# Kernel tuning notes

Hardware: AMD Instinct MI355X
Metric: run time of the kernel (lower is better)

## Reference

```python
import jax, jax.numpy as jnp
import numpy as np

B = 2_000_000
INPUT_DIM = 2
HIDDEN = 32
HALF = HIDDEN // 2  # 16
N_BUCKETS = 50


def setup_inputs() -> dict:
    key = jax.random.key(0)
    ks = jax.random.split(key, 8)
    x = jax.random.normal(ks[0], (B, INPUT_DIM), dtype=jnp.float32)
    buckets = jax.random.randint(ks[1], (B,), 0, N_BUCKETS)
    # shared MLP params (Linear stores W as [out,in]; we keep [in,out] for einsum)
    W1 = jax.random.normal(ks[2], (INPUT_DIM, HIDDEN), dtype=jnp.float32) * 0.5
    b1 = jax.random.normal(ks[3], (HIDDEN,), dtype=jnp.float32) * 0.1
    W2 = jax.random.normal(ks[4], (HIDDEN, HALF), dtype=jnp.float32) * 0.2
    b2 = jax.random.normal(ks[5], (HALF,), dtype=jnp.float32) * 0.1
    # per-bucket heads: each Linear(HALF, 1) -> stacked [N_BUCKETS, HALF] + [N_BUCKETS]
    Wh = jax.random.normal(ks[6], (N_BUCKETS, HALF), dtype=jnp.float32) * 0.2
    bh = jax.random.normal(ks[7], (N_BUCKETS,), dtype=jnp.float32) * 0.1
    return {"x": x, "buckets": buckets, "W1": W1, "b1": b1, "W2": W2, "b2": b2, "Wh": Wh, "bh": bh}


def reference(x, buckets, W1, b1, W2, b2, Wh, bh):
    # shared MLP: Linear -> ReLU -> Linear
    h = jax.nn.relu(x @ W1 + b1) @ W2 + b2            # [B, HALF]
    # bucket routing with clamp-to-last for out-of-range ids
    ids = jnp.where(buckets < N_BUCKETS, buckets, N_BUCKETS - 1)  # [B]
    w = Wh[ids]                                        # [B, HALF] gather
    out = jnp.einsum('bd,bd->b', h, w) + bh[ids]       # [B]
    return out
```

## Files before the change

kernel.cpp:

```cpp
#include <hip/hip_runtime.h>

#define NB 50
#define BLOCK 256


__device__ __forceinline__ float dot4relu(float x0, float x1,
                                          float4 wa, float4 wb, float4 bb,
                                          float4 v, float acc)
{
    float h;
    h = fmaf(x0, wa.x, fmaf(x1, wb.x, bb.x)); h = fmaxf(h, 0.f); acc = fmaf(h, v.x, acc);
    h = fmaf(x0, wa.y, fmaf(x1, wb.y, bb.y)); h = fmaxf(h, 0.f); acc = fmaf(h, v.y, acc);
    h = fmaf(x0, wa.z, fmaf(x1, wb.z, bb.z)); h = fmaxf(h, 0.f); acc = fmaf(h, v.z, acc);
    h = fmaf(x0, wa.w, fmaf(x1, wb.w, bb.w)); h = fmaxf(h, 0.f); acc = fmaf(h, v.w, acc);
    return acc;
}

__global__ __launch_bounds__(BLOCK) void lightwin_kernel(
    const float4* __restrict__ xq,
    const int4*   __restrict__ bq,
    const float*  __restrict__ W1,
    const float*  __restrict__ b1,
    const float*  __restrict__ W2,
    const float*  __restrict__ b2,
    const float*  __restrict__ Wh,
    const float*  __restrict__ bh,
    float4*       __restrict__ outq,
    int nq)
{
    __shared__ float sV[NB * 32];
    __shared__ float sc[NB];

    for (int t = threadIdx.x; t < NB * 32; t += BLOCK) {
        int id = t >> 5;
        int k  = t & 31;
        float s = 0.f;
        #pragma unroll
        for (int j = 0; j < 16; ++j)
            s = fmaf(W2[(k << 4) + j], Wh[(id << 4) + j], s);
        sV[(id << 5) | (((((unsigned)k >> 2) ^ (unsigned)id) & 7u) << 2) | (k & 3)] = s;
    }
    for (int t = threadIdx.x; t < NB; t += BLOCK) {
        float s = bh[t];
        #pragma unroll
        for (int j = 0; j < 16; ++j)
            s = fmaf(b2[j], Wh[(t << 4) + j], s);
        sc[t] = s;
    }
    __syncthreads();

    int tid = blockIdx.x * BLOCK + threadIdx.x;
    if (tid >= nq) return;

    float4 xa = xq[2 * tid];
    float4 xb = xq[2 * tid + 1];
    int4 ib = bq[tid];
    int id0 = ib.x < NB ? ib.x : NB - 1;
    int id1 = ib.y < NB ? ib.y : NB - 1;
    int id2 = ib.z < NB ? ib.z : NB - 1;
    int id3 = ib.w < NB ? ib.w : NB - 1;

    const float4* sV4 = (const float4*)sV;
    const float4* W14 = (const float4*)W1;
    const float4* b14 = (const float4*)b1;

    float acc0 = sc[id0];
    float acc1 = sc[id1];
    float acc2 = sc[id2];
    float acc3 = sc[id3];

    #pragma unroll
    for (int kb = 0; kb < 8; ++kb) {
        float4 wa = W14[kb];
        float4 wb = W14[8 + kb];
        float4 bb = b14[kb];
        float4 v0 = sV4[(id0 << 3) | (((unsigned)(kb ^ id0)) & 7u)];
        float4 v1 = sV4[(id1 << 3) | (((unsigned)(kb ^ id1)) & 7u)];
        float4 v2 = sV4[(id2 << 3) | (((unsigned)(kb ^ id2)) & 7u)];
        float4 v3 = sV4[(id3 << 3) | (((unsigned)(kb ^ id3)) & 7u)];
        acc0 = dot4relu(xa.x, xa.y, wa, wb, bb, v0, acc0);
        acc1 = dot4relu(xa.z, xa.w, wa, wb, bb, v1, acc1);
        acc2 = dot4relu(xb.x, xb.y, wa, wb, bb, v2, acc2);
        acc3 = dot4relu(xb.z, xb.w, wa, wb, bb, v3, acc3);
    }

    float4 o; o.x = acc0; o.y = acc1; o.z = acc2; o.w = acc3;
    outq[tid] = o;
}

extern "C" void kernel_launch(void* const* d_in, const int* in_sizes, int n_in,
                              void* d_out, int out_size, void* d_ws, size_t ws_size,
                              hipStream_t stream) {
    const float* x       = (const float*)d_in[0];
    const int*   buckets = (const int*)d_in[1];
    const float* W1      = (const float*)d_in[2];
    const float* b1      = (const float*)d_in[3];
    const float* W2      = (const float*)d_in[4];
    const float* b2      = (const float*)d_in[5];
    const float* Wh      = (const float*)d_in[6];
    const float* bh      = (const float*)d_in[7];
    float* out = (float*)d_out;

    int B  = in_sizes[1];
    int nq = B / 4;
    int grid = (nq + BLOCK - 1) / BLOCK;

    lightwin_kernel<<<grid, BLOCK, 0, stream>>>(
        (const float4*)x, (const int4*)buckets, W1, b1, W2, b2, Wh, bh,
        (float4*)out, nq);
}
```

Before: 97.80 us.

## Precompute fused head weights in a separate kernel and stage via workspace

Moves the per-block recomputation of W2·Wh and b2·Wh+bh into a small precompute kernel that writes to workspace. The main kernel then copies the 1664 floats into shared memory with float4 loads. It also issues the x and bucket loads before the barrier so their latency overlaps the staging, and changes the LDS swizzle hash. This removes redundant FMA work in each of roughly 2000 blocks, at the cost of an extra kernel launch and a global read per block.

```diff
diff --git a/kernel.cpp b/kernel.cpp
--- a/kernel.cpp
+++ b/kernel.cpp
@@ -3,6 +3,33 @@
 #define NB 50
 #define BLOCK 256
 
+
+__global__ __launch_bounds__(BLOCK) void precompute_kernel(
+    const float* __restrict__ W2,
+    const float* __restrict__ b2,
+    const float* __restrict__ Wh,
+    const float* __restrict__ bh,
+    float*       __restrict__ ws)
+{
+    int t = blockIdx.x * BLOCK + threadIdx.x;
+    if (t < NB * 32) {
+        int id = t >> 5;
+        int k  = t & 31;
+        float s = 0.f;
+        #pragma unroll
+        for (int j = 0; j < 16; ++j)
+            s = fmaf(W2[(k << 4) + j], Wh[(id << 4) + j], s);
+        int h = (id + (id >> 3)) & 7;
+        ws[(id << 5) | ((((k >> 2) ^ h) & 7) << 2) | (k & 3)] = s;
+    } else if (t < NB * 32 + NB) {
+        int id = t - NB * 32;
+        float s = bh[id];
+        #pragma unroll
+        for (int j = 0; j < 16; ++j)
+            s = fmaf(b2[j], Wh[(id << 4) + j], s);
+        ws[NB * 32 + id] = s;
+    }
+}
 
 __device__ __forceinline__ float dot4relu(float x0, float x1,
                                           float4 wa, float4 wb, float4 bb,
@@ -21,46 +48,42 @@
     const int4*   __restrict__ bq,
     const float*  __restrict__ W1,
     const float*  __restrict__ b1,
-    const float*  __restrict__ W2,
-    const float*  __restrict__ b2,
-    const float*  __restrict__ Wh,
-    const float*  __restrict__ bh,
+    const float4* __restrict__ wsq,
     float4*       __restrict__ outq,
     int nq)
 {
-    __shared__ float sV[NB * 32];
-    __shared__ float sc[NB];
+    __shared__ float sVc[416 * 4];
 
-    for (int t = threadIdx.x; t < NB * 32; t += BLOCK) {
-        int id = t >> 5;
-        int k  = t & 31;
-        float s = 0.f;
-        #pragma unroll
-        for (int j = 0; j < 16; ++j)
-            s = fmaf(W2[(k << 4) + j], Wh[(id << 4) + j], s);
-        sV[(id << 5) | (((((unsigned)k >> 2) ^ (unsigned)id) & 7u) << 2) | (k & 3)] = s;
+    int tid = blockIdx.x * BLOCK + threadIdx.x;
+    bool active = tid < nq;
+
+    float4 xa = {}, xb = {};
+    int4 ib = {};
+    if (active) {
+        xa = xq[2 * tid];
+        xb = xq[2 * tid + 1];
+        ib = bq[tid];
     }
-    for (int t = threadIdx.x; t < NB; t += BLOCK) {
-        float s = bh[t];
-        #pragma unroll
-        for (int j = 0; j < 16; ++j)
-            s = fmaf(b2[j], Wh[(t << 4) + j], s);
-        sc[t] = s;
-    }
+
+    float4* sq = (float4*)sVc;
+    #pragma unroll
+    for (int t = threadIdx.x; t < 416; t += BLOCK)
+        sq[t] = wsq[t];
     __syncthreads();
 
-    int tid = blockIdx.x * BLOCK + threadIdx.x;
-    if (tid >= nq) return;
+    if (!active) return;
 
-    float4 xa = xq[2 * tid];
-    float4 xb = xq[2 * tid + 1];
-    int4 ib = bq[tid];
     int id0 = ib.x < NB ? ib.x : NB - 1;
     int id1 = ib.y < NB ? ib.y : NB - 1;
     int id2 = ib.z < NB ? ib.z : NB - 1;
     int id3 = ib.w < NB ? ib.w : NB - 1;
+    int h0 = (id0 + (id0 >> 3)) & 7;
+    int h1 = (id1 + (id1 >> 3)) & 7;
+    int h2 = (id2 + (id2 >> 3)) & 7;
+    int h3 = (id3 + (id3 >> 3)) & 7;
 
-    const float4* sV4 = (const float4*)sV;
+    const float4* sV4 = (const float4*)sVc;
+    const float*  sc  = sVc + NB * 32;
     const float4* W14 = (const float4*)W1;
     const float4* b14 = (const float4*)b1;
 
@@ -74,10 +97,10 @@
         float4 wa = W14[kb];
         float4 wb = W14[8 + kb];
         float4 bb = b14[kb];
-        float4 v0 = sV4[(id0 << 3) | (((unsigned)(kb ^ id0)) & 7u)];
-        float4 v1 = sV4[(id1 << 3) | (((unsigned)(kb ^ id1)) & 7u)];
-        float4 v2 = sV4[(id2 << 3) | (((unsigned)(kb ^ id2)) & 7u)];
-        float4 v3 = sV4[(id3 << 3) | (((unsigned)(kb ^ id3)) & 7u)];
+        float4 v0 = sV4[(id0 << 3) | ((kb ^ h0) & 7)];
+        float4 v1 = sV4[(id1 << 3) | ((kb ^ h1) & 7)];
+        float4 v2 = sV4[(id2 << 3) | ((kb ^ h2) & 7)];
+        float4 v3 = sV4[(id3 << 3) | ((kb ^ h3) & 7)];
         acc0 = dot4relu(xa.x, xa.y, wa, wb, bb, v0, acc0);
         acc1 = dot4relu(xa.z, xa.w, wa, wb, bb, v1, acc1);
         acc2 = dot4relu(xb.x, xb.y, wa, wb, bb, v2, acc2);
@@ -100,12 +123,16 @@
     const float* Wh      = (const float*)d_in[6];
     const float* bh      = (const float*)d_in[7];
     float* out = (float*)d_out;
+    float* ws  = (float*)d_ws;
 
     int B  = in_sizes[1];
     int nq = B / 4;
+
+    precompute_kernel<<<(NB * 32 + NB + BLOCK - 1) / BLOCK, BLOCK, 0, stream>>>(
+        W2, b2, Wh, bh, ws);
+
     int grid = (nq + BLOCK - 1) / BLOCK;
-
     lightwin_kernel<<<grid, BLOCK, 0, stream>>>(
-        (const float4*)x, (const int4*)buckets, W1, b1, W2, b2, Wh, bh,
-        (float4*)out, nq);
+        (const float4*)x, (const int4*)buckets, W1, b1,
+        (const float4*)ws, (float4*)out, nq);
 }
```

Result: faster. 89.86 us (-8.1%).
